# Performance work log

Measured on AMD Instinct MI355X. Metric: run time of the kernel, lower is better.

Reference implementation:

```python
import jax, jax.numpy as jnp
import numpy as np
from jax import lax

B, S, F, H, V, T = 64, 1024, 128, 512, 64, 64
SOS, EOS = 0, 1


def lstm_cell(x, h, c, W_ih, W_hh, b_ih, b_hh):
    # PyTorch LSTM gate order: i, f, g, o
    gates = x @ W_ih.T + h @ W_hh.T + b_ih + b_hh  # [B, 4H]
    i, f, g, o = jnp.split(gates, 4, axis=-1)
    c_new = jax.nn.sigmoid(f) * c + jax.nn.sigmoid(i) * jnp.tanh(g)
    h_new = jax.nn.sigmoid(o) * jnp.tanh(c_new)
    return h_new, c_new


def setup_inputs() -> dict:
    key = jax.random.key(0)
    ks = jax.random.split(key, 12)
    s = 0.05  # weight scale to avoid gate saturation
    return {
        "signal": jax.random.normal(ks[0], (B, S, F), jnp.float32),
        "target": jax.random.randint(ks[1], (B, T), 0, V),
        "enc_W_ih": jax.random.normal(ks[2], (4 * H, F), jnp.float32) * s,
        "enc_W_hh": jax.random.normal(ks[3], (4 * H, H), jnp.float32) * s,
        "enc_b_ih": jax.random.normal(ks[4], (4 * H,), jnp.float32) * s,
        "enc_b_hh": jax.random.normal(ks[5], (4 * H,), jnp.float32) * s,
        "dec_W_ih": jax.random.normal(ks[6], (4 * H, V), jnp.float32) * s,
        "dec_W_hh": jax.random.normal(ks[7], (4 * H, H), jnp.float32) * s,
        "dec_b_ih": jax.random.normal(ks[8], (4 * H,), jnp.float32) * s,
        "dec_b_hh": jax.random.normal(ks[9], (4 * H,), jnp.float32) * s,
        "out_W": jax.random.normal(ks[10], (V, H), jnp.float32) * s,
        "out_b": jax.random.normal(ks[11], (V,), jnp.float32) * s,
    }


def reference(signal, target, enc_W_ih, enc_W_hh, enc_b_ih, enc_b_hh,
              dec_W_ih, dec_W_hh, dec_b_ih, dec_b_hh, out_W, out_b):
    b = signal.shape[0]
    hdim = enc_W_hh.shape[1]
    vocab = out_b.shape[0]
    n_steps = target.shape[1]  # max_loop = target.size(1)

    # ---- encoder LSTM (only final hidden state is used downstream) ----
    def enc_step(carry, x_t):
        h, c = carry
        h, c = lstm_cell(x_t, h, c, enc_W_ih, enc_W_hh, enc_b_ih, enc_b_hh)
        return (h, c), None

    h0 = jnp.zeros((b, hdim), signal.dtype)
    (h, c), _ = lax.scan(enc_step, (h0, h0), jnp.swapaxes(signal, 0, 1))

    # ---- decoder: teacher-start (one-hot target[:,0]) then greedy feedback ----
    inp0 = jax.nn.one_hot(target[:, 0], vocab, dtype=signal.dtype)  # [B, V]

    def dec_step(carry, _):
        h, c, x = carry
        x = jax.nn.relu(x)  # F.relu on one-hot input (faithful to source)
        h, c = lstm_cell(x, h, c, dec_W_ih, dec_W_hh, dec_b_ih, dec_b_hh)
        logits = h @ out_W.T + out_b  # [B, V]
        nxt = jax.nn.one_hot(jnp.argmax(logits, axis=-1), vocab, dtype=x.dtype)
        return (h, c, nxt), logits

    (_, _, _), logits = lax.scan(dec_step, (h, c, inp0), None, length=n_steps)
    logits = jnp.swapaxes(logits, 0, 1)  # [B, T, V]
    return jax.nn.log_softmax(logits, axis=-1)
```

## Files before the change

### kernel.cpp

```cpp
#include <hip/hip_runtime.h>
#include <cstddef>
#include <math.h>

#define NGROUP 4
#define WPG    32
#define NWG    128
#define BPG    16
#define HH  512
#define TT  64
#define VV  64
#define FF  128
#define SS  1024

typedef _Float16 f16;
typedef _Float16 f16x8 __attribute__((ext_vector_type(8)));
typedef float    f32x4 __attribute__((ext_vector_type(4)));
typedef unsigned int u32;
typedef unsigned short u16;
typedef u32 u32x4 __attribute__((ext_vector_type(4)));
typedef unsigned long long u64;

#define C1 4.8828125e-4f
#define C2 2.384185791015625e-7f

__device__ __forceinline__ void split8(const float* __restrict__ p, f16x8& hi, f16x8& lo) {
  f32x4 u = *(const f32x4*)p;
  f32x4 v = *(const f32x4*)(p + 4);
#pragma unroll
  for (int j = 0; j < 4; ++j) {
    f16 a = (f16)u[j]; hi[j]   = a; lo[j]   = (f16)((u[j] - (float)a) * 2048.0f);
    f16 b = (f16)v[j]; hi[4+j] = b; lo[4+j] = (f16)((v[j] - (float)b) * 2048.0f);
  }
}
__device__ __forceinline__ float sigmf_(float x) { return 1.0f / (1.0f + expf(-x)); }

__device__ __forceinline__ f32x4 ld16f(const void* p) {
  f32x4 r;
  asm volatile("global_load_dwordx4 %0, %1, off sc0 sc1" : "=v"(r) : "v"(p) : "memory");
  return r;
}
__device__ __forceinline__ void st4f(u32* p, u32 v) {
  __hip_atomic_store(p, v, __ATOMIC_RELAXED, __HIP_MEMORY_SCOPE_AGENT);
}
__device__ __forceinline__ void st4ff(float* p, float v) {
  __hip_atomic_store(p, v, __ATOMIC_RELAXED, __HIP_MEMORY_SCOPE_AGENT);
}
__device__ __forceinline__ u32 ld4f(const u32* p) {
  return __hip_atomic_load(p, __ATOMIC_RELAXED, __HIP_MEMORY_SCOPE_AGENT);
}
__device__ __forceinline__ void arrive(u32* p) {
  __hip_atomic_fetch_add(p, 1u, __ATOMIC_RELAXED, __HIP_MEMORY_SCOPE_AGENT);
}
#define VMWAIT asm volatile("s_waitcnt vmcnt(0)" ::: "memory")

__device__ __forceinline__ void wait_cnt(const u32* cnt, u32 target) {
  while (ld4f(cnt) < target)
    __builtin_amdgcn_s_sleep(1);
}

#define MFMA(d, a, b) d = __builtin_amdgcn_mfma_f32_16x16x32_f16(a, b, d, 0, 0, 0)

#define STAGE_H(src_)                                                         \
  { const u32* src = (src_) + (size_t)(tid >> 4) * 256;                       \
    const int cq_ = tid & 15;                                                 \
    f32x4 sv[4];                                                              \
    _Pragma("unroll") for (int u2 = 0; u2 < 4; ++u2)                          \
      sv[u2] = ld16f(src + cq_*4 + u2*64);                                    \
    VMWAIT;                                                                   \
    _Pragma("unroll") for (int u2 = 0; u2 < 4; ++u2)                          \
      asm volatile("" : "+v"(sv[u2]));                                        \
    __builtin_amdgcn_sched_barrier(0);                                        \
    const int r_ = tid >> 4;                                                  \
    const size_t swz = (size_t)((r_ & 7) << 4);                               \
    _Pragma("unroll") for (int u2 = 0; u2 < 4; ++u2) {                        \
      size_t off = ((size_t)r_*1024 + (size_t)cq_*16 + (size_t)u2*256) ^ swz; \
      *(u32x4*)((char*)sh_h + off) = __builtin_bit_cast(u32x4, sv[u2]);       \
    } }                                                                       \
  __syncthreads();

#define LDA(s, ah)                                                            \
  { size_t o_ = ((size_t)mn * 1024 + (size_t)(s) * 64 + (size_t)(q8 * 2))     \
                ^ (size_t)((mn & 7) << 4);                                    \
    ah = *(const f16x8*)((const char*)sh_h + o_); }

#define HPART()                                                               \
  _Pragma("unroll") for (int s = 0; s < 16; ++s) {                            \
    f16x8 ah; LDA(s, ah);                                                     \
    MFMA(acc0, ah, whh_h[s]);                                                 \
    MFMA(acc1, ah, whh_l[s]);                                                 \
  }

#define XPART(ts)                                                             \
  { acc0 = zero4; acc1 = zero4; acc2 = zero4;                                 \
    const float* sb = sig + (size_t)(gb + mn) * (SS * FF) + (size_t)(ts) * FF;\
    _Pragma("unroll") for (int s = 0; s < 4; ++s) {                           \
      f16x8 xh, xl;                                                           \
      split8(sb + s * 32 + q8, xh, xl);                                       \
      MFMA(acc0, xh, wih_h[s]);                                               \
      MFMA(acc1, xl, wih_h[s]);                                               \
      MFMA(acc1, xh, wih_l[s]);                                               \
      MFMA(acc2, xl, wih_l[s]);                                               \
    } }

#define GWRITE()                                                              \
  _Pragma("unroll") for (int r = 0; r < 4; ++r)                               \
    gate_buf[w][q * 4 + r][mn] = acc0[r] + C1 * acc1[r] + C2 * acc2[r];

#define HSTORE(dst)                                                           \
  { f16 hh = (f16)h;                                                          \
    u32 mine = (u32)__builtin_bit_cast(u16, hh);                              \
    u32 part = (u32)__shfl_xor((int)mine, 1, 64);                             \
    if ((tid & 1) == 0)                                                       \
      st4f((dst) + (size_t)cb * 256 + p * 8 + (ck >> 1), mine | (part << 16)); }

__global__ void __launch_bounds__(256, 1) lstm_seq2seq(
    const float* __restrict__ sig,
    const int*   __restrict__ tgt,
    const float* __restrict__ eWih,
    const float* __restrict__ eWhh,
    const float* __restrict__ eBih,
    const float* __restrict__ eBhh,
    const float* __restrict__ dWih,
    const float* __restrict__ dWhh,
    const float* __restrict__ dBih,
    const float* __restrict__ dBhh,
    const float* __restrict__ oW,
    const float* __restrict__ oB,
    float*       __restrict__ out,
    unsigned char* __restrict__ ws)
{
  const int wg = blockIdx.x;
  const int g  = wg >> 5;
  const int p  = wg & 31;
  const int gb = g * BPG;
  u32* cnt    = (u32*)ws + (size_t)g * 32;
  u32* idxbuf = (u32*)(ws + 16384);
  u32* h16[2] = { (u32*)(ws + 20480) + (size_t)(g*2 + 0) * 4096,
                  (u32*)(ws + 20480) + (size_t)(g*2 + 1) * 4096 };
  float* hfg  = (float*)(ws + 151552) + (size_t)g * 8192;

  const int tid  = threadIdx.x;
  const int w    = tid >> 6;
  const int lane = tid & 63;
  const int q    = lane >> 4;
  const int mn   = lane & 15;
  const int q8   = q * 8;
  const int row  = w * HH + p * 16 + mn;
  const int cb   = tid >> 4;
  const int ck   = tid & 15;
  const int crow = p * 16 + ck;

  __shared__ __attribute__((aligned(16))) f16 sh_h[16 * 512];
  __shared__ float gate_buf[4][16][17];
  __shared__ float bias_buf[4][16];
  __shared__ __attribute__((aligned(16))) float hrow[512];
  __shared__ double psum[64];

  f16x8 whh_h[16], whh_l[16], wih_h[4], wih_l[4];
#pragma unroll
  for (int s = 0; s < 16; ++s)
    split8(eWhh + (size_t)row * HH + s * 32 + q8, whh_h[s], whh_l[s]);
#pragma unroll
  for (int s = 0; s < 4; ++s)
    split8(eWih + (size_t)row * FF + s * 32 + q8, wih_h[s], wih_l[s]);
  if (tid < 64) {
    int g4 = tid >> 4, kl = tid & 15;
    int r = g4 * HH + p * 16 + kl;
    bias_buf[g4][kl] = eBih[r] + eBhh[r];
  }
  if (p == 0 && tid < BPG)
    st4f(idxbuf + gb + tid, (u32)tgt[(size_t)(gb + tid) * TT]);
  __syncthreads();

  float c_reg = 0.f;
  int cur = 0;
  const f32x4 zero4 = {0.f, 0.f, 0.f, 0.f};
  f32x4 acc0, acc1, acc2;

  XPART(0)
  for (int t = 0; t < SS; ++t) {
    wait_cnt(cnt, 32u * (u32)t);
    STAGE_H(h16[cur])
    HPART()
    GWRITE()
    __syncthreads();
    {
      float gi = gate_buf[0][cb][ck] + bias_buf[0][ck];
      float gf = gate_buf[1][cb][ck] + bias_buf[1][ck];
      float gg = gate_buf[2][cb][ck] + bias_buf[2][ck];
      float go = gate_buf[3][cb][ck] + bias_buf[3][ck];
      float c  = sigmf_(gf) * c_reg + sigmf_(gi) * tanhf(gg);
      float h  = sigmf_(go) * tanhf(c);
      c_reg = c;
      HSTORE(h16[cur ^ 1])
    }
    XPART(t + 1 < SS ? t + 1 : SS - 1)
    VMWAIT;
    __syncthreads();
    if (tid == 0) arrive(cnt);
    cur ^= 1;
  }

#pragma unroll
  for (int s = 0; s < 16; ++s)
    split8(dWhh + (size_t)row * HH + s * 32 + q8, whh_h[s], whh_l[s]);
  __syncthreads();
  if (tid < 64) {
    int g4 = tid >> 4, kl = tid & 15;
    int r = g4 * HH + p * 16 + kl;
    bias_buf[g4][kl] = dBih[r] + dBhh[r];
  }
  __syncthreads();

  for (int t = 0; t < TT; ++t) {
    wait_cnt(cnt, 32u * (u32)(SS + 2 * t));
    acc0 = zero4; acc1 = zero4; acc2 = zero4;
    STAGE_H(h16[cur])
    HPART()
    GWRITE()
    __syncthreads();
    {
      int ib = (int)ld4f(idxbuf + gb + cb);
      float gi = gate_buf[0][cb][ck] + bias_buf[0][ck] + dWih[(size_t)(0*HH + crow) * VV + ib];
      float gf = gate_buf[1][cb][ck] + bias_buf[1][ck] + dWih[(size_t)(1*HH + crow) * VV + ib];
      float gg = gate_buf[2][cb][ck] + bias_buf[2][ck] + dWih[(size_t)(2*HH + crow) * VV + ib];
      float go = gate_buf[3][cb][ck] + bias_buf[3][ck] + dWih[(size_t)(3*HH + crow) * VV + ib];
      float c  = sigmf_(gf) * c_reg + sigmf_(gi) * tanhf(gg);
      float h  = sigmf_(go) * tanhf(c);
      c_reg = c;
      HSTORE(h16[cur ^ 1])
      st4ff(hfg + (size_t)cb * HH + crow, h);
    }
    VMWAIT;
    __syncthreads();
    if (tid == 0) arrive(cnt);
    int nxt = cur ^ 1;

    wait_cnt(cnt, 32u * (u32)(SS + 2 * t + 1));
    if (p < BPG) {
      if (tid < 128) {
        f32x4 hv = ld16f(hfg + (size_t)p * HH + tid * 4);
        VMWAIT;
        *(f32x4*)&hrow[tid * 4] = hv;
      }
      __syncthreads();
      double acc = 0.0;
      if (w < 2) {
        const float* wr = oW + (size_t)lane * HH + w * 256;
        const float* hr = hrow + w * 256;
#pragma unroll 4
        for (int kc = 0; kc < 64; ++kc) {
          f32x4 hv = *(const f32x4*)(hr + kc * 4);
          f32x4 wv = *(const f32x4*)(wr + kc * 4);
          acc += (double)hv[0]*(double)wv[0] + (double)hv[1]*(double)wv[1]
               + (double)hv[2]*(double)wv[2] + (double)hv[3]*(double)wv[3];
        }
        if (w == 1) psum[lane] = acc;
      }
      __syncthreads();
      if (w == 0) {
        double l = acc + psum[lane] + (double)oB[lane];
        double mx = l; int ai = lane;
#pragma unroll
        for (int o = 32; o > 0; o >>= 1) {
          double om = __shfl_xor(mx, o, 64);
          int    oi = __shfl_xor(ai, o, 64);
          if (om > mx || (om == mx && oi < ai)) { mx = om; ai = oi; }
        }
        double se = exp(l - mx);
#pragma unroll
        for (int o = 32; o > 0; o >>= 1) se += __shfl_xor(se, o, 64);
        double lse = mx + log(se);
        out[((size_t)(gb + p) * TT + t) * VV + lane] = (float)(l - lse);
        if (lane == 0) st4f(idxbuf + gb + p, (u32)ai);
      }
    }
    VMWAIT;
    __syncthreads();
    if (tid == 0) arrive(cnt);
    cur = nxt;
  }
}

extern "C" void kernel_launch(void* const* d_in, const int* in_sizes, int n_in,
                              void* d_out, int out_size, void* d_ws, size_t ws_size,
                              hipStream_t stream) {
  (void)in_sizes; (void)n_in; (void)out_size; (void)ws_size;
  hipMemsetAsync(d_ws, 0, 151552, stream);
  lstm_seq2seq<<<dim3(NWG), dim3(256), 0, stream>>>(
      (const float*)d_in[0],  (const int*)d_in[1],
      (const float*)d_in[2],  (const float*)d_in[3],
      (const float*)d_in[4],  (const float*)d_in[5],
      (const float*)d_in[6],  (const float*)d_in[7],
      (const float*)d_in[8],  (const float*)d_in[9],
      (const float*)d_in[10], (const float*)d_in[11],
      (float*)d_out, (unsigned char*)d_ws);
}
```

Measured before the change: 5.927 ms.

## Replace counter barriers with step-tagged 64-bit data words for inter-block sync

Removes the global atomic arrival counter and spin-wait. Each published h value, h-row entry and argmax index now carries its timestep tag in the upper 32 bits of a 64-bit store, and consumers poll the data itself until all tags match. The next step's h loads are issued early, before the input projection work, so their latency overlaps compute. This cuts a full-grid barrier round trip per step. In exchange it doubles the bytes moved for h and makes consumers re-poll on tag mismatch, with memory-ordering risk resting on 64-bit store atomicity.

```diff
diff --git a/kernel.cpp b/kernel.cpp
--- a/kernel.cpp
+++ b/kernel.cpp
@@ -17,7 +17,7 @@
 typedef float    f32x4 __attribute__((ext_vector_type(4)));
 typedef unsigned int u32;
 typedef unsigned short u16;
-typedef u32 u32x4 __attribute__((ext_vector_type(4)));
+typedef u32 u32x2 __attribute__((ext_vector_type(2)));
 typedef unsigned long long u64;
 
 #define C1 4.8828125e-4f
@@ -39,42 +39,50 @@
   asm volatile("global_load_dwordx4 %0, %1, off sc0 sc1" : "=v"(r) : "v"(p) : "memory");
   return r;
 }
-__device__ __forceinline__ void st4f(u32* p, u32 v) {
+__device__ __forceinline__ u64 ld8f(const u64* p) {
+  u64 r;
+  asm volatile("global_load_dwordx2 %0, %1, off sc0 sc1" : "=v"(r) : "v"(p) : "memory");
+  return r;
+}
+__device__ __forceinline__ void st8f(u64* p, u64 v) {
   __hip_atomic_store(p, v, __ATOMIC_RELAXED, __HIP_MEMORY_SCOPE_AGENT);
 }
-__device__ __forceinline__ void st4ff(float* p, float v) {
-  __hip_atomic_store(p, v, __ATOMIC_RELAXED, __HIP_MEMORY_SCOPE_AGENT);
-}
-__device__ __forceinline__ u32 ld4f(const u32* p) {
-  return __hip_atomic_load(p, __ATOMIC_RELAXED, __HIP_MEMORY_SCOPE_AGENT);
-}
-__device__ __forceinline__ void arrive(u32* p) {
-  __hip_atomic_fetch_add(p, 1u, __ATOMIC_RELAXED, __HIP_MEMORY_SCOPE_AGENT);
-}
 #define VMWAIT asm volatile("s_waitcnt vmcnt(0)" ::: "memory")
 
-__device__ __forceinline__ void wait_cnt(const u32* cnt, u32 target) {
-  while (ld4f(cnt) < target)
-    __builtin_amdgcn_s_sleep(1);
-}
-
 #define MFMA(d, a, b) d = __builtin_amdgcn_mfma_f32_16x16x32_f16(a, b, d, 0, 0, 0)
 
-#define STAGE_H(src_)                                                         \
-  { const u32* src = (src_) + (size_t)(tid >> 4) * 256;                       \
-    const int cq_ = tid & 15;                                                 \
-    f32x4 sv[4];                                                              \
-    _Pragma("unroll") for (int u2 = 0; u2 < 4; ++u2)                          \
-      sv[u2] = ld16f(src + cq_*4 + u2*64);                                    \
+#define STAGE_ISSUE(src_)                                                     \
+  _Pragma("unroll") for (int u2 = 0; u2 < 8; ++u2)                            \
+    sv[u2] = ld16f((src_) + (size_t)(tid >> 4) * 256                          \
+                   + (size_t)((tid & 15) * 2 + u2 * 32));
+
+#define STAGE_WAIT(src_, tg)                                                  \
+  for (;;) {                                                                  \
     VMWAIT;                                                                   \
-    _Pragma("unroll") for (int u2 = 0; u2 < 4; ++u2)                          \
+    _Pragma("unroll") for (int u2 = 0; u2 < 8; ++u2)                          \
       asm volatile("" : "+v"(sv[u2]));                                        \
     __builtin_amdgcn_sched_barrier(0);                                        \
-    const int r_ = tid >> 4;                                                  \
+    u32 badv[8]; u32 anyb = 0;                                                \
+    _Pragma("unroll") for (int u2 = 0; u2 < 8; ++u2) {                        \
+      union { f32x4 f; u32 u4[4]; } U; U.f = sv[u2];                          \
+      badv[u2] = (U.u4[1] ^ (u32)(tg)) | (U.u4[3] ^ (u32)(tg));               \
+      anyb |= badv[u2];                                                       \
+    }                                                                         \
+    if (__all(anyb == 0)) break;                                              \
+    __builtin_amdgcn_s_sleep(1);                                              \
+    _Pragma("unroll") for (int u2 = 0; u2 < 8; ++u2)                          \
+      if (badv[u2])                                                           \
+        sv[u2] = ld16f((src_) + (size_t)(tid >> 4) * 256                      \
+                       + (size_t)((tid & 15) * 2 + u2 * 32));                 \
+  }
+
+#define STAGE_WRITE()                                                         \
+  { const int r_ = tid >> 4, cq_ = tid & 15;                                  \
     const size_t swz = (size_t)((r_ & 7) << 4);                               \
-    _Pragma("unroll") for (int u2 = 0; u2 < 4; ++u2) {                        \
-      size_t off = ((size_t)r_*1024 + (size_t)cq_*16 + (size_t)u2*256) ^ swz; \
-      *(u32x4*)((char*)sh_h + off) = __builtin_bit_cast(u32x4, sv[u2]);       \
+    _Pragma("unroll") for (int u2 = 0; u2 < 8; ++u2) {                        \
+      union { f32x4 f; u32 u4[4]; } U; U.f = sv[u2];                          \
+      size_t off = ((size_t)r_*1024 + (size_t)cq_*8 + (size_t)u2*128) ^ swz;  \
+      *(u32x2*)((char*)sh_h + off) = (u32x2){U.u4[0], U.u4[2]};               \
     } }                                                                       \
   __syncthreads();
 
@@ -106,12 +114,12 @@
   _Pragma("unroll") for (int r = 0; r < 4; ++r)                               \
     gate_buf[w][q * 4 + r][mn] = acc0[r] + C1 * acc1[r] + C2 * acc2[r];
 
-#define HSTORE(dst)                                                           \
-  { f16 hh = (f16)h;                                                          \
-    u32 mine = (u32)__builtin_bit_cast(u16, hh);                              \
+#define HSTORE64(dst, tg)                                                     \
+  { u32 mine = (u32)__builtin_bit_cast(u16, (f16)h);                          \
     u32 part = (u32)__shfl_xor((int)mine, 1, 64);                             \
     if ((tid & 1) == 0)                                                       \
-      st4f((dst) + (size_t)cb * 256 + p * 8 + (ck >> 1), mine | (part << 16)); }
+      st8f((dst) + (size_t)cb * 256 + p * 8 + (ck >> 1),                      \
+           (u64)(mine | (part << 16)) | ((u64)(u32)(tg) << 32)); }
 
 __global__ void __launch_bounds__(256, 1) lstm_seq2seq(
     const float* __restrict__ sig,
@@ -129,15 +137,15 @@
     float*       __restrict__ out,
     unsigned char* __restrict__ ws)
 {
+  u64* idx64 = (u64*)ws;
+  u64* h16[2] = { (u64*)(ws + 4096) + (size_t)((blockIdx.x >> 5)*2 + 0) * 4096,
+                  (u64*)(ws + 4096) + (size_t)((blockIdx.x >> 5)*2 + 1) * 4096 };
+  u64* hfg   = (u64*)(ws + 266240) + (size_t)(blockIdx.x >> 5) * 8192;
+
   const int wg = blockIdx.x;
   const int g  = wg >> 5;
   const int p  = wg & 31;
   const int gb = g * BPG;
-  u32* cnt    = (u32*)ws + (size_t)g * 32;
-  u32* idxbuf = (u32*)(ws + 16384);
-  u32* h16[2] = { (u32*)(ws + 20480) + (size_t)(g*2 + 0) * 4096,
-                  (u32*)(ws + 20480) + (size_t)(g*2 + 1) * 4096 };
-  float* hfg  = (float*)(ws + 151552) + (size_t)g * 8192;
 
   const int tid  = threadIdx.x;
   const int w    = tid >> 6;
@@ -169,18 +177,20 @@
     bias_buf[g4][kl] = eBih[r] + eBhh[r];
   }
   if (p == 0 && tid < BPG)
-    st4f(idxbuf + gb + tid, (u32)tgt[(size_t)(gb + tid) * TT]);
+    st8f(idx64 + gb + tid,
+         (u64)(u32)tgt[(size_t)(gb + tid) * TT] | (1ull << 32));
   __syncthreads();
 
   float c_reg = 0.f;
-  int cur = 0;
   const f32x4 zero4 = {0.f, 0.f, 0.f, 0.f};
   f32x4 acc0, acc1, acc2;
-
+  f32x4 sv[8];
+
+  STAGE_ISSUE(h16[0])
   XPART(0)
   for (int t = 0; t < SS; ++t) {
-    wait_cnt(cnt, 32u * (u32)t);
-    STAGE_H(h16[cur])
+    STAGE_WAIT(h16[t & 1], t)
+    STAGE_WRITE()
     HPART()
     GWRITE()
     __syncthreads();
@@ -192,19 +202,17 @@
       float c  = sigmf_(gf) * c_reg + sigmf_(gi) * tanhf(gg);
       float h  = sigmf_(go) * tanhf(c);
       c_reg = c;
-      HSTORE(h16[cur ^ 1])
+      HSTORE64(h16[(t + 1) & 1], t + 1)
     }
+    STAGE_ISSUE(h16[(t + 1) & 1])
     XPART(t + 1 < SS ? t + 1 : SS - 1)
-    VMWAIT;
-    __syncthreads();
-    if (tid == 0) arrive(cnt);
-    cur ^= 1;
-  }
+  }
+
+  __syncthreads();
 
 #pragma unroll
   for (int s = 0; s < 16; ++s)
     split8(dWhh + (size_t)row * HH + s * 32 + q8, whh_h[s], whh_l[s]);
-  __syncthreads();
   if (tid < 64) {
     int g4 = tid >> 4, kl = tid & 15;
     int r = g4 * HH + p * 16 + kl;
@@ -213,14 +221,25 @@
   __syncthreads();
 
   for (int t = 0; t < TT; ++t) {
-    wait_cnt(cnt, 32u * (u32)(SS + 2 * t));
+    STAGE_ISSUE(h16[(SS + t) & 1])
+    const u64* iap = idx64 + gb + cb;
+    u64 iv = ld8f(iap);
     acc0 = zero4; acc1 = zero4; acc2 = zero4;
-    STAGE_H(h16[cur])
+    STAGE_WAIT(h16[(SS + t) & 1], SS + t)
+    STAGE_WRITE()
     HPART()
     GWRITE()
     __syncthreads();
     {
-      int ib = (int)ld4f(idxbuf + gb + cb);
+      for (;;) {
+        asm volatile("" : "+v"(iv));
+        __builtin_amdgcn_sched_barrier(0);
+        if ((u32)(iv >> 32) == (u32)(t + 1)) break;
+        __builtin_amdgcn_s_sleep(1);
+        iv = ld8f(iap);
+        VMWAIT;
+      }
+      int ib = (int)(u32)iv;
       float gi = gate_buf[0][cb][ck] + bias_buf[0][ck] + dWih[(size_t)(0*HH + crow) * VV + ib];
       float gf = gate_buf[1][cb][ck] + bias_buf[1][ck] + dWih[(size_t)(1*HH + crow) * VV + ib];
       float gg = gate_buf[2][cb][ck] + bias_buf[2][ck] + dWih[(size_t)(2*HH + crow) * VV + ib];
@@ -228,20 +247,31 @@
       float c  = sigmf_(gf) * c_reg + sigmf_(gi) * tanhf(gg);
       float h  = sigmf_(go) * tanhf(c);
       c_reg = c;
-      HSTORE(h16[cur ^ 1])
-      st4ff(hfg + (size_t)cb * HH + crow, h);
+      HSTORE64(h16[(SS + t + 1) & 1], SS + t + 1)
+      st8f(hfg + (size_t)cb * HH + crow,
+           (u64)__builtin_bit_cast(u32, h) | ((u64)(u32)(SS + t + 1) << 32));
     }
-    VMWAIT;
-    __syncthreads();
-    if (tid == 0) arrive(cnt);
-    int nxt = cur ^ 1;
-
-    wait_cnt(cnt, 32u * (u32)(SS + 2 * t + 1));
+
     if (p < BPG) {
+      const u32 tg = (u32)(SS + t + 1);
       if (tid < 128) {
-        f32x4 hv = ld16f(hfg + (size_t)p * HH + tid * 4);
-        VMWAIT;
-        *(f32x4*)&hrow[tid * 4] = hv;
+        const u64* hp = hfg + (size_t)p * HH + (size_t)tid * 4;
+        f32x4 a = ld16f(hp), b2 = ld16f(hp + 2);
+        for (;;) {
+          VMWAIT;
+          asm volatile("" : "+v"(a), "+v"(b2));
+          __builtin_amdgcn_sched_barrier(0);
+          union { f32x4 f; u32 u4[4]; } A, B2; A.f = a; B2.f = b2;
+          u32 bad = (A.u4[1]^tg) | (A.u4[3]^tg) | (B2.u4[1]^tg) | (B2.u4[3]^tg);
+          if (__all(bad == 0)) break;
+          __builtin_amdgcn_s_sleep(1);
+          a = ld16f(hp); b2 = ld16f(hp + 2);
+        }
+        union { f32x4 f; u32 u4[4]; } A, B2; A.f = a; B2.f = b2;
+        hrow[tid*4+0] = __builtin_bit_cast(float, A.u4[0]);
+        hrow[tid*4+1] = __builtin_bit_cast(float, A.u4[2]);
+        hrow[tid*4+2] = __builtin_bit_cast(float, B2.u4[0]);
+        hrow[tid*4+3] = __builtin_bit_cast(float, B2.u4[2]);
       }
       __syncthreads();
       double acc = 0.0;
@@ -272,13 +302,11 @@
         for (int o = 32; o > 0; o >>= 1) se += __shfl_xor(se, o, 64);
         double lse = mx + log(se);
         out[((size_t)(gb + p) * TT + t) * VV + lane] = (float)(l - lse);
-        if (lane == 0) st4f(idxbuf + gb + p, (u32)ai);
+        if (lane == 0)
+          st8f(idx64 + gb + p, (u64)(u32)ai | ((u64)(u32)(t + 2) << 32));
       }
     }
-    VMWAIT;
     __syncthreads();
-    if (tid == 0) arrive(cnt);
-    cur = nxt;
   }
 }
 
@@ -286,7 +314,7 @@
                               void* d_out, int out_size, void* d_ws, size_t ws_size,
                               hipStream_t stream) {
   (void)in_sizes; (void)n_in; (void)out_size; (void)ws_size;
-  hipMemsetAsync(d_ws, 0, 151552, stream);
+  hipMemsetAsync(d_ws, 0, 528384, stream);
   lstm_seq2seq<<<dim3(NWG), dim3(256), 0, stream>>>(
       (const float*)d_in[0],  (const int*)d_in[1],
       (const float*)d_in[2],  (const float*)d_in[3],
```

Measured after the change: 5.804 ms. 2.1% less time.
